# Optimization experiments

Hardware: AMD Instinct MI355X
Metric: run time of the kernel (lower is better)

The kernel has to match this reference:

```python
import jax, jax.numpy as jnp
import numpy as np

L_ORDER = 1
R_ORDER = 1
THRESHOLD = 1.0


def setup_inputs() -> dict:
    key = jax.random.key(0)
    k0, k1, k2, k3, k4 = jax.random.split(key, 5)
    B, T, D, K = 16, 2048, 512, L_ORDER + R_ORDER + 1
    hidden = jax.random.normal(k0, (B, T, D), jnp.float32)
    conv_w = jax.random.normal(k1, (D, 1, K), jnp.float32) / np.sqrt(K).astype(np.float32)
    conv_b = jax.random.normal(k2, (D,), jnp.float32) * 0.05
    lin_w = jax.random.normal(k3, (1, D), jnp.float32) / np.sqrt(D).astype(np.float32)
    lin_b = jax.random.normal(k4, (1,), jnp.float32) * 0.05
    return {"hidden": hidden, "conv_w": conv_w, "conv_b": conv_b, "lin_w": lin_w, "lin_b": lin_b}


def _alphas(hidden, conv_w, conv_b, lin_w, lin_b):
    # hidden: [B, T, D]
    ctx = jnp.transpose(hidden, (0, 2, 1))              # [B, D, T]
    q = jnp.pad(ctx, ((0, 0), (0, 0), (L_ORDER, R_ORDER)))
    mem = jax.lax.conv_general_dilated(
        q, conv_w, (1,), 'VALID',
        dimension_numbers=('NCH', 'OIH', 'NCH'),
        feature_group_count=ctx.shape[1]) + conv_b[None, :, None]   # depthwise conv
    out = jax.nn.relu(jnp.transpose(mem + ctx, (0, 2, 1)))          # [B, T, D] (dropout = identity in eval)
    logits = out @ lin_w.T + lin_b                                  # [B, T, 1]
    return jax.nn.sigmoid(logits)[..., 0]                           # [B, T]


def _cif_scan(hidden, alphas):
    # Sequential integrate-and-fire recurrence over time via lax.scan.
    B, T, H = hidden.shape

    def step(carry, xs):
        integ, frame = carry        # [B], [B, H]
        a, h = xs                   # [B], [B, H]
        dist = 1.0 - integ
        integ = integ + a
        fire_out = integ            # recorded pre-reset (matches torch list_fires)
        fire = integ >= THRESHOLD
        integ = jnp.where(fire, integ - 1.0, integ)
        cur = jnp.where(fire, dist, a)
        rem = a - cur
        frame_out = frame + cur[:, None] * h   # recorded pre-reset
        frame = jnp.where(fire[:, None], rem[:, None] * h, frame_out)
        return (integ, frame), (fire_out, frame_out)

    init = (jnp.zeros((B,), hidden.dtype), jnp.zeros((B, H), hidden.dtype))
    _, (fires, frames) = jax.lax.scan(
        step, init, (alphas.T, jnp.transpose(hidden, (1, 0, 2))))
    return jnp.transpose(fires, (1, 0)), jnp.transpose(frames, (1, 0, 2))  # [B,T], [B,T,H]


def reference(hidden, conv_w, conv_b, lin_w, lin_b):
    B, T, H = hidden.shape
    alphas = _alphas(hidden, conv_w, conv_b, lin_w, lin_b)   # [B, T]
    token_num = alphas.sum(-1)                               # [B]
    fires, frames = _cif_scan(hidden, alphas)
    # Ragged extraction: gather frames at fire positions, left-packed, zero-padded
    # to max_label_len = max(round(sum alphas)). Data-dependent length -> python int.
    max_label_len = int(jnp.max(jnp.round(token_num)))
    fire_mask = fires >= THRESHOLD                           # [B, T]
    rank = jnp.cumsum(fire_mask, axis=1) - 1                 # output slot per fire
    b_idx = jnp.arange(B)[:, None]
    vals = jnp.where(fire_mask[..., None], frames, 0.0)
    acoustic_embeds = jnp.zeros((B, max_label_len, H), hidden.dtype)
    acoustic_embeds = acoustic_embeds.at[b_idx, rank].add(vals, mode='drop')
    return acoustic_embeds, token_num, alphas, fires
```

## Files before the change

### kernel.cpp

```cpp
#include <hip/hip_runtime.h>
#include <math.h>

#define B_ 16
#define T_ 2048
#define D_ 512


__global__ __launch_bounds__(256) void k_alphas(
    const float* __restrict__ hidden,
    const float* __restrict__ conv_w,
    const float* __restrict__ conv_b,
    const float* __restrict__ lin_w,
    const float* __restrict__ lin_b,
    float* __restrict__ alpha_ws,
    float* __restrict__ alphas_out)
{
    const int wid  = blockIdx.x * 4 + (threadIdx.x >> 6);
    const int lane = threadIdx.x & 63;
    const int t    = wid & (T_ - 1);
    const float* rowc = hidden + (size_t)wid * D_ + lane * 8;

    float hm[8], hc[8], hp[8];
    {
        float4 x = ((const float4*)rowc)[0], y = ((const float4*)rowc)[1];
        hc[0]=x.x; hc[1]=x.y; hc[2]=x.z; hc[3]=x.w;
        hc[4]=y.x; hc[5]=y.y; hc[6]=y.z; hc[7]=y.w;
    }
    if (t > 0) {
        float4 x = ((const float4*)(rowc - D_))[0], y = ((const float4*)(rowc - D_))[1];
        hm[0]=x.x; hm[1]=x.y; hm[2]=x.z; hm[3]=x.w;
        hm[4]=y.x; hm[5]=y.y; hm[6]=y.z; hm[7]=y.w;
    } else {
        for (int i = 0; i < 8; ++i) hm[i] = 0.f;
    }
    if (t < T_ - 1) {
        float4 x = ((const float4*)(rowc + D_))[0], y = ((const float4*)(rowc + D_))[1];
        hp[0]=x.x; hp[1]=x.y; hp[2]=x.z; hp[3]=x.w;
        hp[4]=y.x; hp[5]=y.y; hp[6]=y.z; hp[7]=y.w;
    } else {
        for (int i = 0; i < 8; ++i) hp[i] = 0.f;
    }

    float dot = 0.f;
    #pragma unroll
    for (int i = 0; i < 8; ++i) {
        int d = lane * 8 + i;
        float mem = hm[i] * conv_w[3 * d] + hc[i] * conv_w[3 * d + 1]
                  + hp[i] * conv_w[3 * d + 2] + conv_b[d];
        float o = mem + hc[i];
        o = o > 0.f ? o : 0.f;
        dot += o * lin_w[d];
    }
    #pragma unroll
    for (int off = 32; off > 0; off >>= 1) dot += __shfl_down(dot, off);

    if (lane == 0) {
        float a = 1.f / (1.f + expf(-(dot + lin_b[0])));
        alpha_ws[wid]  = a;
        alphas_out[wid] = a;
    }
}

__global__ __launch_bounds__(256) void k_scan(
    const float* __restrict__ alpha_ws,
    double* __restrict__ S,
    int*    __restrict__ fire_pos,
    int*    __restrict__ n_fires,
    float*  __restrict__ fires_out,
    float*  __restrict__ token_out)
{
    const int b = blockIdx.x, tid = threadIdx.x;
    const size_t base = (size_t)b * T_;

    double a[8], tsum = 0.0;
    #pragma unroll
    for (int i = 0; i < 8; ++i) { a[i] = (double)alpha_ws[base + tid * 8 + i]; tsum += a[i]; }

    __shared__ double ssum[256];
    ssum[tid] = tsum;
    __syncthreads();
    for (int off = 1; off < 256; off <<= 1) {
        double v = (tid >= off) ? ssum[tid - off] : 0.0;
        __syncthreads();
        ssum[tid] += v;
        __syncthreads();
    }
    double run = ssum[tid] - tsum;

    #pragma unroll
    for (int i = 0; i < 8; ++i) {
        int t = tid * 8 + i;
        double Sp = run, fp = floor(Sp);
        run += a[i];
        S[base + t] = run;
        fires_out[base + t] = (float)(run - fp);
        if (run >= fp + 1.0) fire_pos[base + (long long)fp] = t;
    }
    if (tid == 255) {
        n_fires[b]   = (int)floor(run);
        token_out[b] = (float)run;
    }
}

__global__ __launch_bounds__(256) void k_gather(
    const float*  __restrict__ hidden,
    const double* __restrict__ S,
    const int*    __restrict__ fire_pos,
    const int*    __restrict__ n_fires,
    float* __restrict__ acoustic, int ML)
{
    const int s = blockIdx.x, b = blockIdx.y;
    float2* dst = (float2*)(acoustic + ((size_t)b * ML + s) * D_) + threadIdx.x;

    int nf = n_fires[b];
    if (nf > ML) nf = ML;
    if (s >= nf) { *dst = make_float2(0.f, 0.f); return; }

    const size_t base = (size_t)b * T_;
    const int t_end   = fire_pos[base + s];
    const int t_start = (s == 0) ? 0 : fire_pos[base + s - 1];

    const double vlo = (double)s, vhi = (double)(s + 1);
    float acc0 = 0.f, acc1 = 0.f;
    double Sp = (t_start == 0) ? 0.0 : S[base + t_start - 1];
    const float* hrow = hidden + (base + (size_t)t_start) * D_ + threadIdx.x * 2;
    for (int t = t_start; t <= t_end; ++t, hrow += D_) {
        double St = S[base + t];
        double wd = fmin(St, vhi) - fmax(Sp, vlo);
        float w = wd > 0.0 ? (float)wd : 0.f;
        float2 hv = *(const float2*)hrow;
        acc0 += w * hv.x;
        acc1 += w * hv.y;
        Sp = St;
    }
    *dst = make_float2(acc0, acc1);
}

extern "C" void kernel_launch(void* const* d_in, const int* in_sizes, int n_in,
                              void* d_out, int out_size, void* d_ws, size_t ws_size,
                              hipStream_t stream) {
    (void)in_sizes; (void)n_in; (void)ws_size;
    const float* hidden = (const float*)d_in[0];
    const float* conv_w = (const float*)d_in[1];
    const float* conv_b = (const float*)d_in[2];
    const float* lin_w  = (const float*)d_in[3];
    const float* lin_b  = (const float*)d_in[4];

    const int B = B_, T = T_, D = D_;
    int ML = (out_size - (B + 2 * B * T)) / (B * D);
    if (ML < 1) ML = 1;

    float* out        = (float*)d_out;
    float* acoustic   = out;
    float* token_out  = out + (size_t)B * ML * D;
    float* alphas_out = token_out + B;
    float* fires_out  = alphas_out + (size_t)B * T;

    double* S        = (double*)d_ws;
    float*  alpha_ws = (float*)(S + (size_t)B * T);
    int*    fire_pos = (int*)(alpha_ws + (size_t)B * T);
    int*    n_fires  = fire_pos + (size_t)B * T;

    k_alphas<<<B * T / 4, 256, 0, stream>>>(hidden, conv_w, conv_b, lin_w,
                                            lin_b, alpha_ws, alphas_out);
    k_scan<<<B, 256, 0, stream>>>(alpha_ws, S, fire_pos, n_fires,
                                  fires_out, token_out);
    k_gather<<<dim3(ML, B), 256, 0, stream>>>(hidden, S, fire_pos, n_fires,
                                              acoustic, ML);
}
```

Baseline: 139.5 us.

## Process 16 timesteps per wave in alphas kernel with sliding row window

Each wave in the alphas kernel now handles 16 consecutive timesteps with a rolling three-row register window. Each hidden row is loaded about once per wave instead of three times, and the conv and linear weights are held in registers across iterations. The separate alpha workspace copy is dropped, so the scan reads alphas straight from the output buffer. The cost is fewer blocks in flight and a serial dependency within each wave's loop.

```diff
diff --git a/kernel.cpp b/kernel.cpp
--- a/kernel.cpp
+++ b/kernel.cpp
@@ -12,57 +12,69 @@
     const float* __restrict__ conv_b,
     const float* __restrict__ lin_w,
     const float* __restrict__ lin_b,
-    float* __restrict__ alpha_ws,
     float* __restrict__ alphas_out)
 {
-    const int wid  = blockIdx.x * 4 + (threadIdx.x >> 6);
+    const int b    = blockIdx.y;
+    const int wv   = threadIdx.x >> 6;
     const int lane = threadIdx.x & 63;
-    const int t    = wid & (T_ - 1);
-    const float* rowc = hidden + (size_t)wid * D_ + lane * 8;
+    const int t0   = blockIdx.x * 64 + wv * 16;
+    const int d0   = lane * 8;
 
-    float hm[8], hc[8], hp[8];
-    {
-        float4 x = ((const float4*)rowc)[0], y = ((const float4*)rowc)[1];
-        hc[0]=x.x; hc[1]=x.y; hc[2]=x.z; hc[3]=x.w;
-        hc[4]=y.x; hc[5]=y.y; hc[6]=y.z; hc[7]=y.w;
-    }
-    if (t > 0) {
-        float4 x = ((const float4*)(rowc - D_))[0], y = ((const float4*)(rowc - D_))[1];
-        hm[0]=x.x; hm[1]=x.y; hm[2]=x.z; hm[3]=x.w;
-        hm[4]=y.x; hm[5]=y.y; hm[6]=y.z; hm[7]=y.w;
-    } else {
-        for (int i = 0; i < 8; ++i) hm[i] = 0.f;
-    }
-    if (t < T_ - 1) {
-        float4 x = ((const float4*)(rowc + D_))[0], y = ((const float4*)(rowc + D_))[1];
-        hp[0]=x.x; hp[1]=x.y; hp[2]=x.z; hp[3]=x.w;
-        hp[4]=y.x; hp[5]=y.y; hp[6]=y.z; hp[7]=y.w;
-    } else {
-        for (int i = 0; i < 8; ++i) hp[i] = 0.f;
-    }
-
-    float dot = 0.f;
+    float w0[8], w1[8], w2[8], cb[8], lw[8];
     #pragma unroll
     for (int i = 0; i < 8; ++i) {
-        int d = lane * 8 + i;
-        float mem = hm[i] * conv_w[3 * d] + hc[i] * conv_w[3 * d + 1]
-                  + hp[i] * conv_w[3 * d + 2] + conv_b[d];
-        float o = mem + hc[i];
-        o = o > 0.f ? o : 0.f;
-        dot += o * lin_w[d];
+        int d = d0 + i;
+        w0[i] = conv_w[3 * d];
+        w1[i] = conv_w[3 * d + 1];
+        w2[i] = conv_w[3 * d + 2];
+        cb[i] = conv_b[d];
+        lw[i] = lin_w[d];
     }
-    #pragma unroll
-    for (int off = 32; off > 0; off >>= 1) dot += __shfl_down(dot, off);
+    const float lb = lin_b[0];
 
-    if (lane == 0) {
-        float a = 1.f / (1.f + expf(-(dot + lin_b[0])));
-        alpha_ws[wid]  = a;
-        alphas_out[wid] = a;
+    const float* rbase = hidden + (size_t)b * T_ * D_ + d0;
+    auto loadrow = [&](int t, float* f) {
+        const float4* p = (const float4*)(rbase + (size_t)t * D_);
+        float4 x = p[0], y = p[1];
+        f[0]=x.x; f[1]=x.y; f[2]=x.z; f[3]=x.w;
+        f[4]=y.x; f[5]=y.y; f[6]=y.z; f[7]=y.w;
+    };
+
+    float hm[8], hc[8], hp[8], nx[8];
+    if (t0 > 0) { loadrow(t0 - 1, hm); }
+    else        { for (int i = 0; i < 8; ++i) hm[i] = 0.f; }
+    loadrow(t0, hc);
+    loadrow(t0 + 1, hp);
+
+    float* aout = alphas_out + (size_t)b * T_;
+    #pragma unroll 4
+    for (int j = 0; j < 16; ++j) {
+        const int t = t0 + j;
+        const int tn = t + 2;
+        if (tn < T_) { loadrow(tn, nx); }
+        else         { for (int i = 0; i < 8; ++i) nx[i] = 0.f; }
+
+        float dot = 0.f;
+        #pragma unroll
+        for (int i = 0; i < 8; ++i) {
+            float mem = fmaf(hm[i], w0[i],
+                        fmaf(hc[i], w1[i],
+                        fmaf(hp[i], w2[i], cb[i])));
+            float o = mem + hc[i];
+            o = o > 0.f ? o : 0.f;
+            dot += o * lw[i];
+        }
+        #pragma unroll
+        for (int off = 32; off > 0; off >>= 1) dot += __shfl_down(dot, off);
+        if (lane == 0) aout[t] = 1.f / (1.f + expf(-(dot + lb)));
+
+        #pragma unroll
+        for (int i = 0; i < 8; ++i) { hm[i] = hc[i]; hc[i] = hp[i]; hp[i] = nx[i]; }
     }
 }
 
 __global__ __launch_bounds__(256) void k_scan(
-    const float* __restrict__ alpha_ws,
+    const float* __restrict__ alphas_in,
     double* __restrict__ S,
     int*    __restrict__ fire_pos,
     int*    __restrict__ n_fires,
@@ -74,7 +86,7 @@
 
     double a[8], tsum = 0.0;
     #pragma unroll
-    for (int i = 0; i < 8; ++i) { a[i] = (double)alpha_ws[base + tid * 8 + i]; tsum += a[i]; }
+    for (int i = 0; i < 8; ++i) { a[i] = (double)alphas_in[base + tid * 8 + i]; tsum += a[i]; }
 
     __shared__ double ssum[256];
     ssum[tid] = tsum;
@@ -157,13 +169,12 @@
     float* fires_out  = alphas_out + (size_t)B * T;
 
     double* S        = (double*)d_ws;
-    float*  alpha_ws = (float*)(S + (size_t)B * T);
-    int*    fire_pos = (int*)(alpha_ws + (size_t)B * T);
+    int*    fire_pos = (int*)(S + (size_t)B * T);
     int*    n_fires  = fire_pos + (size_t)B * T;
 
-    k_alphas<<<B * T / 4, 256, 0, stream>>>(hidden, conv_w, conv_b, lin_w,
-                                            lin_b, alpha_ws, alphas_out);
-    k_scan<<<B, 256, 0, stream>>>(alpha_ws, S, fire_pos, n_fires,
+    k_alphas<<<dim3(T / 64, B), 256, 0, stream>>>(hidden, conv_w, conv_b,
+                                                  lin_w, lin_b, alphas_out);
+    k_scan<<<B, 256, 0, stream>>>(alphas_out, S, fire_pos, n_fires,
                                   fires_out, token_out);
     k_gather<<<dim3(ML, B), 256, 0, stream>>>(hidden, S, fire_pos, n_fires,
                                               acoustic, ML);
```

Result: faster. 132.7 us (-4.9%).
